# Performance work log

Measured on AMD Instinct MI355X. Metric: run time of the kernel, lower is better.

Reference implementation:

```python
import jax, jax.numpy as jnp
import numpy as np

B, S, D, H = 2, 2048, 1024, 16
DK = D // H

def setup_inputs() -> dict:
    key = jax.random.key(0)
    ks = jax.random.split(key, 8)
    return {
        "query": jax.random.normal(ks[0], (B, S, D), dtype=jnp.float32),
        "key": jax.random.normal(ks[1], (B, S, D), dtype=jnp.float32),
        "value": jax.random.normal(ks[2], (B, S, D), dtype=jnp.float32),
        "mask": jax.random.randint(ks[3], (B, S, S), 0, 2, dtype=jnp.int32),
        "w_q": jax.random.normal(ks[4], (D, D), dtype=jnp.float32) * (D ** -0.5),
        "w_k": jax.random.normal(ks[5], (D, D), dtype=jnp.float32) * (D ** -0.5),
        "w_v": jax.random.normal(ks[6], (D, D), dtype=jnp.float32) * (D ** -0.5),
        "w_o": jax.random.normal(ks[7], (D, D), dtype=jnp.float32) * (D ** -0.5),
    }

def reference(query, key, value, mask, w_q, w_k, w_v, w_o):
    b, s, d = query.shape
    # Linear projections (torch nn.Linear: x @ W.T); here w_* are [out, in]
    Q = jnp.einsum('bsd,ed->bse', query, w_q).reshape(b, s, H, DK).transpose(0, 2, 1, 3)
    K = jnp.einsum('bsd,ed->bse', key, w_k).reshape(b, s, H, DK).transpose(0, 2, 1, 3)
    V = jnp.einsum('bsd,ed->bse', value, w_v).reshape(b, s, H, DK).transpose(0, 2, 1, 3)
    scale = jnp.float32(DK ** 0.5)
    scores = jnp.einsum('bhqd,bhkd->bhqk', Q, K) / scale  # [B,H,S,S]
    scores = jnp.where(mask[:, None, :, :] == 0, jnp.float32(-1e9), scores)
    attn = jax.nn.softmax(scores, axis=-1)  # dropout p=0 -> identity
    out = jnp.einsum('bhqk,bhkd->bhqd', attn, V)  # [B,H,S,DK]
    out = out.transpose(0, 2, 1, 3).reshape(b, s, d)
    return jnp.einsum('bsd,ed->bse', out, w_o)
```

## Files before the change

kernel.cpp:

```cpp
#include <hip/hip_runtime.h>
#include <stdint.h>

#define B_ 2
#define S_ 2048
#define D_ 1024
#define H_ 16
#define DK_ 64

typedef __attribute__((ext_vector_type(8))) short short8;
typedef __attribute__((ext_vector_type(4))) float f32x4;

__device__ __forceinline__ short f2bf(float f) {
    uint32_t u = __float_as_uint(f);
    return (short)((u + 0x7FFFu + ((u >> 16) & 1u)) >> 16);
}

__device__ __forceinline__ float fexp2(float x) {
    float r;
    asm("v_exp_f32 %0, %1" : "=v"(r) : "v"(x));
    return r;
}

__device__ __forceinline__ uint32_t cvt_pk_bf16(float lo, float hi) {
    uint32_t r;
    asm("v_cvt_pk_bf16_f32 %0, %1, %2" : "=v"(r) : "v"(lo), "v"(hi));
    return r;
}

#define GLOAD16(gptr, lptr)                                                      \
    __builtin_amdgcn_global_load_lds(                                            \
        (const __attribute__((address_space(1))) void*)(gptr),                   \
        (__attribute__((address_space(3))) void*)(lptr), 16, 0, 0)

__global__ __launch_bounds__(256) void prep(const float* __restrict__ q,
                                            const float* __restrict__ k,
                                            const float* __restrict__ v,
                                            const float* __restrict__ wq,
                                            const float* __restrict__ wk,
                                            const float* __restrict__ wv,
                                            const float* __restrict__ wo,
                                            const int* __restrict__ mask,
                                            short* __restrict__ qb, short* __restrict__ kb,
                                            short* __restrict__ vb,
                                            short* __restrict__ wqb, short* __restrict__ wkb,
                                            short* __restrict__ wvb, short* __restrict__ wob,
                                            uint32_t* __restrict__ packed,
                                            float* __restrict__ lut) {
    int bid = blockIdx.x;
    int tid = threadIdx.x;
    if (bid < 8192) {
        const float* in;
        short* out;
        int i;
        if (bid < 6144) {
            int sel = bid >> 11;
            i = (bid & 2047) * 256 + tid;
            in = (sel == 0) ? q : (sel == 1) ? k : v;
            out = (sel == 0) ? qb : (sel == 1) ? kb : vb;
        } else {
            int idx = bid - 6144;
            int sel = idx >> 9;
            i = (idx & 511) * 256 + tid;
            in = (sel == 0) ? wq : (sel == 1) ? wk : (sel == 2) ? wv : wo;
            out = (sel == 0) ? wqb : (sel == 1) ? wkb : (sel == 2) ? wvb : wob;
            if (idx == 0 && tid < 64) {
                int e = tid >> 2, r = tid & 3;
                lut[tid] = ((e >> r) & 1) ? 0.0f : -8.0e9f;
            }
        }
        const float4* p = ((const float4*)in) + (size_t)i * 2;
        float4 x = p[0], y = p[1];
        short8 o;
        o[0] = f2bf(x.x); o[1] = f2bf(x.y); o[2] = f2bf(x.z); o[3] = f2bf(x.w);
        o[4] = f2bf(y.x); o[5] = f2bf(y.y); o[6] = f2bf(y.z); o[7] = f2bf(y.w);
        *(((short8*)out) + i) = o;
    } else {
        size_t t = (size_t)(bid - 8192) * 256 + tid;
        int4 m = ((const int4*)mask)[t];
        uint32_t nib = (m.x != 0 ? 1u : 0u) | (m.y != 0 ? 2u : 0u) |
                       (m.z != 0 ? 4u : 0u) | (m.w != 0 ? 8u : 0u);
        int lane = tid & 63;
        uint32_t vv = nib << ((lane & 7) * 4);
        vv |= __shfl_xor(vv, 1);
        vv |= __shfl_xor(vv, 2);
        vv |= __shfl_xor(vv, 4);
        if ((lane & 7) == 0) packed[t >> 3] = vv;
    }
}

#define GEMM_BODY(A, W, C, F32OUT, Mv, Nv, Kv)                                              \
    __shared__ short As[128 * 32];                                                          \
    __shared__ short Bs[128 * 32];                                                          \
    const int tid = threadIdx.x;                                                            \
    const int lane = tid & 63;                                                              \
    const int w = tid >> 6;                                                                 \
    const int wm = w >> 1, wn = w & 1;                                                      \
    const int l_ = blockIdx.x + (blockIdx.y << 3);                                          \
    const int xcd_ = l_ & 7, ii_ = l_ >> 3;                                                 \
    const int mBase = ((xcd_ << 2) + (ii_ >> 3)) * 128;                                     \
    const int nBase = (ii_ & 7) * 128;                                                      \
    f32x4 acc[4][4];                                                                        \
    _Pragma("unroll") for (int i = 0; i < 4; i++)                                           \
        _Pragma("unroll") for (int j = 0; j < 4; j++) acc[i][j] = (f32x4)0.f;               \
    const int srow = lane >> 2;                                                             \
    const int sslot = lane & 3;                                                             \
    for (int k0 = 0; k0 < Kv; k0 += 32) {                                                   \
        _Pragma("unroll") for (int i = 0; i < 2; ++i) {                                     \
            int seg = w * 2 + i;                                                            \
            int row = seg * 16 + srow;                                                      \
            const short* ga = A + (size_t)(mBase + row) * Kv + k0 + sslot * 8;              \
            GLOAD16(ga, (char*)As + seg * 1024);                                            \
            const short* gb = W + (size_t)(nBase + row) * Kv + k0 + sslot * 8;              \
            GLOAD16(gb, (char*)Bs + seg * 1024);                                            \
        }                                                                                   \
        asm volatile("s_waitcnt vmcnt(0)" ::: "memory");                                    \
        __syncthreads();                                                                    \
        short8 af[4], bfv[4];                                                               \
        _Pragma("unroll") for (int mi = 0; mi < 4; mi++)                                    \
            af[mi] = *(const short8*)&As[(wm * 64 + mi * 16 + (lane & 15)) * 32 + (lane >> 4) * 8]; \
        _Pragma("unroll") for (int ni = 0; ni < 4; ni++)                                    \
            bfv[ni] = *(const short8*)&Bs[(wn * 64 + ni * 16 + (lane & 15)) * 32 + (lane >> 4) * 8]; \
        _Pragma("unroll") for (int mi = 0; mi < 4; mi++)                                    \
            _Pragma("unroll") for (int ni = 0; ni < 4; ni++)                                \
                acc[mi][ni] = __builtin_amdgcn_mfma_f32_16x16x32_bf16(af[mi], bfv[ni], acc[mi][ni], 0, 0, 0); \
        __syncthreads();                                                                    \
    }                                                                                       \
    _Pragma("unroll") for (int mi = 0; mi < 4; mi++)                                        \
        _Pragma("unroll") for (int ni = 0; ni < 4; ni++)                                    \
            _Pragma("unroll") for (int r = 0; r < 4; r++) {                                 \
                int row = mBase + wm * 64 + mi * 16 + (lane >> 4) * 4 + r;                  \
                int col = nBase + wn * 64 + ni * 16 + (lane & 15);                          \
                float v = acc[mi][ni][r];                                                   \
                if (F32OUT) ((float*)C)[(size_t)row * Nv + col] = v;                        \
                else        ((short*)C)[(size_t)row * Nv + col] = f2bf(v);                  \
            }

__global__ __launch_bounds__(256) void gemm3_nt(const short* __restrict__ A0, const short* __restrict__ W0, short* __restrict__ C0,
                                                const short* __restrict__ A1, const short* __restrict__ W1, short* __restrict__ C1,
                                                const short* __restrict__ A2, const short* __restrict__ W2, short* __restrict__ C2) {
    const int z = blockIdx.z;
    const short* A = (z == 0) ? A0 : (z == 1) ? A1 : A2;
    const short* W = (z == 0) ? W0 : (z == 1) ? W1 : W2;
    short* C = (z == 0) ? C0 : (z == 1) ? C1 : C2;
    GEMM_BODY(A, W, C, 0, (B_ * S_), D_, D_)
}

__global__ __launch_bounds__(256) void gemm_out(const short* __restrict__ A,
                                                const short* __restrict__ W,
                                                float* __restrict__ C) {
    GEMM_BODY(A, W, C, 1, (B_ * S_), D_, D_)
}

__global__ __launch_bounds__(256) void transpose_v(const short* __restrict__ Vp,
                                                   short* __restrict__ Vt) {
    __shared__ short t[64 * 72];
    int bid = blockIdx.x;
    int bh = bid >> 5;
    int st = bid & 31;
    int b = bh >> 4, h = bh & 15;
    int sBase = st * 64;
    int tid = threadIdx.x;
#pragma unroll
    for (int i = 0; i < 2; i++) {
        int ci = i * 256 + tid;
        int sr = ci >> 3, sl = ci & 7;
        short8 v = *(const short8*)&Vp[(size_t)(b * S_ + sBase + sr) * D_ + h * 64 + sl * 8];
#pragma unroll
        for (int j = 0; j < 8; j++) t[(sl * 8 + j) * 72 + sr] = v[j];
    }
    __syncthreads();
#pragma unroll
    for (int i = 0; i < 2; i++) {
        int ci = i * 256 + tid;
        int dk = ci >> 3, sl = ci & 7;
        short8 o = *(const short8*)&t[dk * 72 + sl * 8];
        *(short8*)&Vt[(size_t)((b * H_ + h) * 64 + dk) * S_ + sBase + sl * 8] = o;
    }
}

__global__ __launch_bounds__(256) void attn_kernel(const short* __restrict__ Qp,
                                                   const short* __restrict__ Kp,
                                                   const short* __restrict__ Vt,
                                                   const uint32_t* __restrict__ mp,
                                                   const float* __restrict__ lutg,
                                                   short* __restrict__ Op) {
    __shared__ short Ks[2][2][64 * 64];
    __shared__ short Vs[2][2][64 * 64];
    const int l_ = blockIdx.x + (blockIdx.y << 4);
    const int bh = ((l_ & 7) << 2) + (l_ >> 7);
    const int qt = (l_ >> 3) & 15;
    const int b = bh >> 4, h = bh & 15;
    const int qBase = qt * 128;
    const int tid = threadIdx.x, lane = tid & 63, w = tid >> 6;
    const int lg = lane >> 4;
    const int li = lane & 15;
    const float c1 = 0.18033688011112042f;

    const int qA = qBase + w * 32 + li;
    const int qB = qA + 16;

    short8 qfA[2], qfB[2];
#pragma unroll
    for (int ks = 0; ks < 2; ks++) {
        qfA[ks] = *(const short8*)&Qp[(size_t)(b * S_ + qA) * D_ + h * 64 + lg * 8 + ks * 32];
        qfB[ks] = *(const short8*)&Qp[(size_t)(b * S_ + qB) * D_ + h * 64 + lg * 8 + ks * 32];
    }

    const int r0 = tid >> 3, sl = tid & 7;
    const int gs = sl ^ (r0 & 7);
    const short* kgb = Kp + ((size_t)(b * S_) + r0) * D_ + h * 64 + gs * 8;
    const short* vgb = Vt + ((size_t)bh * 64 + r0) * S_ + gs * 8;
    const uint32_t* mrowA = mp + ((size_t)(b * S_) + qA) * 64;
    const uint32_t* mrowB = mp + ((size_t)(b * S_) + qB) * 64;
    char* ldsK = (char*)&Ks[0][0][0];
    char* ldsV = (char*)&Vs[0][0][0];
    const int woff = w * 1024;

#pragma unroll
    for (int st = 0; st < 2; st++) {
        GLOAD16(kgb + (size_t)(st * 64) * D_, ldsK + st * 8192 + woff);
        GLOAD16(kgb + (size_t)(st * 64 + 32) * D_, ldsK + st * 8192 + 4096 + woff);
        GLOAD16(vgb + st * 64, ldsV + st * 8192 + woff);
        GLOAD16(vgb + st * 64 + (size_t)32 * S_, ldsV + st * 8192 + 4096 + woff);
    }
    uint4 mw4a = *(const uint4*)mrowA;
    uint4 mw4b = *(const uint4*)mrowB;
    asm volatile("s_waitcnt vmcnt(0)" ::: "memory");
    __syncthreads();

    float m_rA = -1e30f, l_rA = 0.f, m_rB = -1e30f, l_rB = 0.f;
    f32x4 accA[4], accB[4];
#pragma unroll
    for (int g = 0; g < 4; g++) { accA[g] = (f32x4)0.f; accB[g] = (f32x4)0.f; }

    int cur = 0;

    for (int kt = 0; kt < S_ / 128; ++kt) {
        uint32_t mwaA[4] = {mw4a.x, mw4a.y, mw4a.z, mw4a.w};
        uint32_t mwaB[4] = {mw4b.x, mw4b.y, mw4b.z, mw4b.w};
        f32x4 mskA[8], mskB[8];
#pragma unroll
        for (int nt = 0; nt < 8; nt++) {
            uint32_t sh = ((nt & 1) << 4) + (lg << 2);
            mskA[nt] = *(const f32x4*)&lutg[((mwaA[nt >> 1] >> sh) & 0xFu) * 4];
            mskB[nt] = *(const f32x4*)&lutg[((mwaB[nt >> 1] >> sh) & 0xFu) * 4];
        }

        uint4 mwnA, mwnB;
        if (kt < S_ / 128 - 1) {
            const int boff = (cur ^ 1) * 16384 + woff;
#pragma unroll
            for (int st = 0; st < 2; st++) {
                const size_t kr = (size_t)((kt + 1) * 128 + st * 64);
                GLOAD16(kgb + kr * D_, ldsK + boff + st * 8192);
                GLOAD16(kgb + (kr + 32) * D_, ldsK + boff + st * 8192 + 4096);
                GLOAD16(vgb + kr, ldsV + boff + st * 8192);
                GLOAD16(vgb + kr + (size_t)32 * S_, ldsV + boff + st * 8192 + 4096);
            }
            mwnA = *(const uint4*)&mrowA[(kt + 1) * 4];
            mwnB = *(const uint4*)&mrowB[(kt + 1) * 4];
        }

        f32x4 scA[8], scB[8];
        __builtin_amdgcn_s_setprio(1);
#pragma unroll
        for (int st = 0; st < 2; st++)
#pragma unroll
            for (int ntl = 0; ntl < 4; ntl++) {
                f32x4 cA = mskA[st * 4 + ntl];
                f32x4 cB = mskB[st * 4 + ntl];
#pragma unroll
                for (int ks = 0; ks < 2; ks++) {
                    short8 kf = *(const short8*)&Ks[cur][st][(ntl * 16 + li) * 64 + (((lg + ks * 4) ^ (li & 7)) << 3)];
                    cA = __builtin_amdgcn_mfma_f32_16x16x32_bf16(kf, qfA[ks], cA, 0, 0, 0);
                    cB = __builtin_amdgcn_mfma_f32_16x16x32_bf16(kf, qfB[ks], cB, 0, 0, 0);
                }
                scA[st * 4 + ntl] = cA;
                scB[st * 4 + ntl] = cB;
            }
        __builtin_amdgcn_s_setprio(0);

        float a0 = fmaxf(fmaxf(scA[0][0], scA[0][1]), fmaxf(scA[0][2], scA[0][3]));
        float a1 = fmaxf(fmaxf(scA[1][0], scA[1][1]), fmaxf(scA[1][2], scA[1][3]));
        float a2 = fmaxf(fmaxf(scA[2][0], scA[2][1]), fmaxf(scA[2][2], scA[2][3]));
        float a3 = fmaxf(fmaxf(scA[3][0], scA[3][1]), fmaxf(scA[3][2], scA[3][3]));
        float a4 = fmaxf(fmaxf(scA[4][0], scA[4][1]), fmaxf(scA[4][2], scA[4][3]));
        float a5 = fmaxf(fmaxf(scA[5][0], scA[5][1]), fmaxf(scA[5][2], scA[5][3]));
        float a6 = fmaxf(fmaxf(scA[6][0], scA[6][1]), fmaxf(scA[6][2], scA[6][3]));
        float a7 = fmaxf(fmaxf(scA[7][0], scA[7][1]), fmaxf(scA[7][2], scA[7][3]));
        float tmA = fmaxf(fmaxf(fmaxf(a0, a1), fmaxf(a2, a3)),
                          fmaxf(fmaxf(a4, a5), fmaxf(a6, a7)));
        tmA = fmaxf(tmA, __shfl_xor(tmA, 16));
        tmA = fmaxf(tmA, __shfl_xor(tmA, 32));
        float b0 = fmaxf(fmaxf(scB[0][0], scB[0][1]), fmaxf(scB[0][2], scB[0][3]));
        float b1 = fmaxf(fmaxf(scB[1][0], scB[1][1]), fmaxf(scB[1][2], scB[1][3]));
        float b2 = fmaxf(fmaxf(scB[2][0], scB[2][1]), fmaxf(scB[2][2], scB[2][3]));
        float b3 = fmaxf(fmaxf(scB[3][0], scB[3][1]), fmaxf(scB[3][2], scB[3][3]));
        float b4 = fmaxf(fmaxf(scB[4][0], scB[4][1]), fmaxf(scB[4][2], scB[4][3]));
        float b5 = fmaxf(fmaxf(scB[5][0], scB[5][1]), fmaxf(scB[5][2], scB[5][3]));
        float b6 = fmaxf(fmaxf(scB[6][0], scB[6][1]), fmaxf(scB[6][2], scB[6][3]));
        float b7 = fmaxf(fmaxf(scB[7][0], scB[7][1]), fmaxf(scB[7][2], scB[7][3]));
        float tmB = fmaxf(fmaxf(fmaxf(b0, b1), fmaxf(b2, b3)),
                          fmaxf(fmaxf(b4, b5), fmaxf(b6, b7)));
        tmB = fmaxf(tmB, __shfl_xor(tmB, 16));
        tmB = fmaxf(tmB, __shfl_xor(tmB, 32));

        if (__any(((tmA - m_rA) * c1 > 10.0f) || ((tmB - m_rB) * c1 > 10.0f))) {
            float mnA = fmaxf(m_rA, tmA);
            float alA = fexp2((m_rA - mnA) * c1);
            m_rA = mnA; l_rA *= alA;
            float mnB = fmaxf(m_rB, tmB);
            float alB = fexp2((m_rB - mnB) * c1);
            m_rB = mnB; l_rB *= alB;
#pragma unroll
            for (int g = 0; g < 4; g++) { accA[g] *= alA; accB[g] *= alB; }
        }
        float mcA = m_rA * c1, mcB = m_rB * c1;

        uint32_t uA[8][2], uB[8][2];
        float lsA = 0.f, lsB = 0.f;
#pragma unroll
        for (int nt = 0; nt < 8; nt++) {
            float e0 = fexp2(__builtin_fmaf(scA[nt][0], c1, -mcA));
            float e1 = fexp2(__builtin_fmaf(scA[nt][1], c1, -mcA));
            float e2 = fexp2(__builtin_fmaf(scA[nt][2], c1, -mcA));
            float e3 = fexp2(__builtin_fmaf(scA[nt][3], c1, -mcA));
            lsA += (e0 + e1) + (e2 + e3);
            uA[nt][0] = cvt_pk_bf16(e0, e1);
            uA[nt][1] = cvt_pk_bf16(e2, e3);
            float f0 = fexp2(__builtin_fmaf(scB[nt][0], c1, -mcB));
            float f1 = fexp2(__builtin_fmaf(scB[nt][1], c1, -mcB));
            float f2 = fexp2(__builtin_fmaf(scB[nt][2], c1, -mcB));
            float f3 = fexp2(__builtin_fmaf(scB[nt][3], c1, -mcB));
            lsB += (f0 + f1) + (f2 + f3);
            uB[nt][0] = cvt_pk_bf16(f0, f1);
            uB[nt][1] = cvt_pk_bf16(f2, f3);
        }
        lsA += __shfl_xor(lsA, 16);
        lsA += __shfl_xor(lsA, 32);
        l_rA += lsA;
        lsB += __shfl_xor(lsB, 16);
        lsB += __shfl_xor(lsB, 32);
        l_rB += lsB;

        __builtin_amdgcn_s_setprio(1);
#pragma unroll
        for (int ks = 0; ks < 4; ks++) {
            const uint32_t sA00 = uA[2 * ks][0], sA01 = uA[2 * ks][1];
            const uint32_t sA10 = uA[2 * ks + 1][0], sA11 = uA[2 * ks + 1][1];
            uint32_t eA0 = (lg & 1) ? sA00 : sA10;
            uint32_t eA1 = (lg & 1) ? sA01 : sA11;
            uint32_t xA0 = (uint32_t)__shfl_xor((int)eA0, 16);
            uint32_t xA1 = (uint32_t)__shfl_xor((int)eA1, 16);
            union { uint32_t w4[4]; short8 s8; } puA;
            puA.w4[0] = (lg & 1) ? xA0 : sA00;
            puA.w4[1] = (lg & 1) ? xA1 : sA01;
            puA.w4[2] = (lg & 1) ? sA10 : xA0;
            puA.w4[3] = (lg & 1) ? sA11 : xA1;
            const uint32_t sB00 = uB[2 * ks][0], sB01 = uB[2 * ks][1];
            const uint32_t sB10 = uB[2 * ks + 1][0], sB11 = uB[2 * ks + 1][1];
            uint32_t eB0 = (lg & 1) ? sB00 : sB10;
            uint32_t eB1 = (lg & 1) ? sB01 : sB11;
            uint32_t xB0 = (uint32_t)__shfl_xor((int)eB0, 16);
            uint32_t xB1 = (uint32_t)__shfl_xor((int)eB1, 16);
            union { uint32_t w4[4]; short8 s8; } puB;
            puB.w4[0] = (lg & 1) ? xB0 : sB00;
            puB.w4[1] = (lg & 1) ? xB1 : sB01;
            puB.w4[2] = (lg & 1) ? sB10 : xB0;
            puB.w4[3] = (lg & 1) ? sB11 : xB1;
            const int f = ks * 4 + ((lg & 1) << 1) + (lg >> 1);
            const int stv = f >> 3, fl = f & 7;
#pragma unroll
            for (int g = 0; g < 4; g++) {
                short8 vf = *(const short8*)&Vs[cur][stv][(g * 16 + li) * 64 + ((fl ^ (li & 7)) << 3)];
                accA[g] = __builtin_amdgcn_mfma_f32_16x16x32_bf16(vf, puA.s8, accA[g], 0, 0, 0);
                accB[g] = __builtin_amdgcn_mfma_f32_16x16x32_bf16(vf, puB.s8, accB[g], 0, 0, 0);
            }
        }
        __builtin_amdgcn_s_setprio(0);

        asm volatile("s_waitcnt vmcnt(0)" ::: "memory");
        __syncthreads();
        cur ^= 1;
        if (kt < S_ / 128 - 1) { mw4a = mwnA; mw4b = mwnB; }
    }

    float invA = 1.f / l_rA, invB = 1.f / l_rB;
    short* orowA = &Op[(size_t)(b * S_ + qA) * D_ + h * 64];
    short* orowB = &Op[(size_t)(b * S_ + qB) * D_ + h * 64];
#pragma unroll
    for (int g = 0; g < 4; g++) {
        uint2 oa, ob;
        oa.x = cvt_pk_bf16(accA[g][0] * invA, accA[g][1] * invA);
        oa.y = cvt_pk_bf16(accA[g][2] * invA, accA[g][3] * invA);
        *(uint2*)&orowA[g * 16 + lg * 4] = oa;
        ob.x = cvt_pk_bf16(accB[g][0] * invB, accB[g][1] * invB);
        ob.y = cvt_pk_bf16(accB[g][2] * invB, accB[g][3] * invB);
        *(uint2*)&orowB[g * 16 + lg * 4] = ob;
    }
}

extern "C" void kernel_launch(void* const* d_in, const int* in_sizes, int n_in,
                              void* d_out, int out_size, void* d_ws, size_t ws_size,
                              hipStream_t stream) {
    const float* q  = (const float*)d_in[0];
    const float* k  = (const float*)d_in[1];
    const float* v  = (const float*)d_in[2];
    const int*   mk = (const int*)d_in[3];
    const float* wq = (const float*)d_in[4];
    const float* wk = (const float*)d_in[5];
    const float* wv = (const float*)d_in[6];
    const float* wo = (const float*)d_in[7];

    const size_t SZ = (size_t)B_ * S_ * D_;
    const size_t DD = (size_t)D_ * D_;
    const size_t NEED = (6 * SZ + 4 * DD) * 2 + (size_t)B_ * S_ * 64 * 4 + 256;
    if (ws_size < NEED) return;

    short* ws  = (short*)d_ws;
    short* qb  = ws;
    short* kb  = qb + SZ;
    short* vb  = kb + SZ;
    short* wqb = vb + SZ;
    short* wkb = wqb + DD;
    short* wvb = wkb + DD;
    short* wob = wvb + DD;
    short* Qp  = wob + DD;
    short* Kp  = Qp + SZ;
    short* Vp  = Kp + SZ;
    uint32_t* mp = (uint32_t*)(Vp + SZ);
    float* lutg = (float*)(mp + (size_t)B_ * S_ * 64);
    short* Vtr = qb;
    short* Opx = kb;

    dim3 blk(256);
    prep<<<dim3(16384), blk, 0, stream>>>(q, k, v, wq, wk, wv, wo, mk,
                                          qb, kb, vb, wqb, wkb, wvb, wob, mp, lutg);

    gemm3_nt<<<dim3(8, 32, 3), blk, 0, stream>>>(qb, wqb, Qp, kb, wkb, Kp, vb, wvb, Vp);

    transpose_v<<<dim3(B_ * H_ * (S_ / 64)), blk, 0, stream>>>(Vp, Vtr);

    attn_kernel<<<dim3(16, 32), dim3(256), 0, stream>>>(Qp, Kp, Vtr, mp, lutg, Opx);

    gemm_out<<<dim3(8, 32), blk, 0, stream>>>(Opx, wob, (float*)d_out);
}
```

Measured before the change: 157.0 us.

## Load V fragments directly from a fragment-ordered global layout instead of via LDS

The V transpose kernel now writes V in a layout already ordered by MFMA fragment, grouped per key tile and fragment index. The attention kernel reads each lane's V operand straight from global memory into registers, ping-ponging between two register sets, and no longer stages V through double-buffered shared memory. This removes the V LDS traffic, halves LDS usage and may raise occupancy. In exchange the V loads now sit inside the compute loop with less latency hiding, and every block re-reads V from global memory or cache.

```diff
diff --git a/kernel.cpp b/kernel.cpp
--- a/kernel.cpp
+++ b/kernel.cpp
@@ -152,13 +152,15 @@
 }
 
 __global__ __launch_bounds__(256) void transpose_v(const short* __restrict__ Vp,
-                                                   short* __restrict__ Vt) {
+                                                   short* __restrict__ Vt2) {
     __shared__ short t[64 * 72];
     int bid = blockIdx.x;
     int bh = bid >> 5;
     int st = bid & 31;
     int b = bh >> 4, h = bh & 15;
     int sBase = st * 64;
+    int kt = st >> 1;
+    int fbase = (st & 1) * 8;
     int tid = threadIdx.x;
 #pragma unroll
     for (int i = 0; i < 2; i++) {
@@ -172,20 +174,19 @@
 #pragma unroll
     for (int i = 0; i < 2; i++) {
         int ci = i * 256 + tid;
-        int dk = ci >> 3, sl = ci & 7;
-        short8 o = *(const short8*)&t[dk * 72 + sl * 8];
-        *(short8*)&Vt[(size_t)((b * H_ + h) * 64 + dk) * S_ + sBase + sl * 8] = o;
+        int fl = ci >> 6, dv = ci & 63;
+        short8 o = *(const short8*)&t[dv * 72 + fl * 8];
+        *(short8*)&Vt2[(size_t)(((bh * 16 + kt) * 16 + fbase + fl) * 64 + dv) * 8] = o;
     }
 }
 
 __global__ __launch_bounds__(256) void attn_kernel(const short* __restrict__ Qp,
                                                    const short* __restrict__ Kp,
-                                                   const short* __restrict__ Vt,
+                                                   const short* __restrict__ Vt2,
                                                    const uint32_t* __restrict__ mp,
                                                    const float* __restrict__ lutg,
                                                    short* __restrict__ Op) {
     __shared__ short Ks[2][2][64 * 64];
-    __shared__ short Vs[2][2][64 * 64];
     const int l_ = blockIdx.x + (blockIdx.y << 4);
     const int bh = ((l_ & 7) << 2) + (l_ >> 7);
     const int qt = (l_ >> 3) & 15;
@@ -209,19 +210,22 @@
     const int r0 = tid >> 3, sl = tid & 7;
     const int gs = sl ^ (r0 & 7);
     const short* kgb = Kp + ((size_t)(b * S_) + r0) * D_ + h * 64 + gs * 8;
-    const short* vgb = Vt + ((size_t)bh * 64 + r0) * S_ + gs * 8;
     const uint32_t* mrowA = mp + ((size_t)(b * S_) + qA) * 64;
     const uint32_t* mrowB = mp + ((size_t)(b * S_) + qB) * 64;
     char* ldsK = (char*)&Ks[0][0][0];
-    char* ldsV = (char*)&Vs[0][0][0];
     const int woff = w * 1024;
+
+    const int flg = ((lg & 1) << 1) + (lg >> 1);
+    const short* v2b = Vt2 + ((size_t)bh * 16) * 8192;
+
+#define LOADV2(dst, ksv, v2k)                                                    \
+    _Pragma("unroll") for (int g = 0; g < 4; g++)                                \
+        dst[g] = *(const short8*)&(v2k)[(((ksv) * 4 + flg) * 64 + g * 16 + li) * 8];
 
 #pragma unroll
     for (int st = 0; st < 2; st++) {
         GLOAD16(kgb + (size_t)(st * 64) * D_, ldsK + st * 8192 + woff);
         GLOAD16(kgb + (size_t)(st * 64 + 32) * D_, ldsK + st * 8192 + 4096 + woff);
-        GLOAD16(vgb + st * 64, ldsV + st * 8192 + woff);
-        GLOAD16(vgb + st * 64 + (size_t)32 * S_, ldsV + st * 8192 + 4096 + woff);
     }
     uint4 mw4a = *(const uint4*)mrowA;
     uint4 mw4b = *(const uint4*)mrowB;
@@ -236,6 +240,11 @@
     int cur = 0;
 
     for (int kt = 0; kt < S_ / 128; ++kt) {
+        const short* v2k = v2b + (size_t)kt * 8192;
+        short8 vA[4], vB[4];
+        LOADV2(vA, 0, v2k);
+        LOADV2(vB, 1, v2k);
+
         uint32_t mwaA[4] = {mw4a.x, mw4a.y, mw4a.z, mw4a.w};
         uint32_t mwaB[4] = {mw4b.x, mw4b.y, mw4b.z, mw4b.w};
         f32x4 mskA[8], mskB[8];
@@ -254,8 +263,6 @@
                 const size_t kr = (size_t)((kt + 1) * 128 + st * 64);
                 GLOAD16(kgb + kr * D_, ldsK + boff + st * 8192);
                 GLOAD16(kgb + (kr + 32) * D_, ldsK + boff + st * 8192 + 4096);
-                GLOAD16(vgb + kr, ldsV + boff + st * 8192);
-                GLOAD16(vgb + kr + (size_t)32 * S_, ldsV + boff + st * 8192 + 4096);
             }
             mwnA = *(const uint4*)&mrowA[(kt + 1) * 4];
             mwnB = *(const uint4*)&mrowB[(kt + 1) * 4];
@@ -368,14 +375,14 @@
             puB.w4[1] = (lg & 1) ? xB1 : sB01;
             puB.w4[2] = (lg & 1) ? sB10 : xB0;
             puB.w4[3] = (lg & 1) ? sB11 : xB1;
-            const int f = ks * 4 + ((lg & 1) << 1) + (lg >> 1);
-            const int stv = f >> 3, fl = f & 7;
 #pragma unroll
             for (int g = 0; g < 4; g++) {
-                short8 vf = *(const short8*)&Vs[cur][stv][(g * 16 + li) * 64 + ((fl ^ (li & 7)) << 3)];
+                short8 vf = (ks & 1) ? vB[g] : vA[g];
                 accA[g] = __builtin_amdgcn_mfma_f32_16x16x32_bf16(vf, puA.s8, accA[g], 0, 0, 0);
                 accB[g] = __builtin_amdgcn_mfma_f32_16x16x32_bf16(vf, puB.s8, accB[g], 0, 0, 0);
             }
+            if (ks == 0) { LOADV2(vA, 2, v2k); }
+            else if (ks == 1) { LOADV2(vB, 3, v2k); }
         }
         __builtin_amdgcn_s_setprio(0);
 
@@ -398,6 +405,7 @@
         ob.y = cvt_pk_bf16(accB[g][2] * invB, accB[g][3] * invB);
         *(uint2*)&orowB[g * 16 + lg * 4] = ob;
     }
+#undef LOADV2
 }
 
 extern "C" void kernel_launch(void* const* d_in, const int* in_sizes, int n_in,
```

Measured after the change: 168.4 us. 1.07x slower.

## Double GEMM K-tile to 64 with XOR-swizzled LDS and defer row-sum reduction

Applied to the files above, without the earlier changes.

The projection GEMM now stages 64-wide K tiles instead of 32, halving the number of load/barrier iterations, and uses an XOR swizzle on the 16-byte LDS slots so the fragment reads avoid bank conflicts. Separately, the attention kernel no longer reduces the per-lane softmax row sums across lane groups on every key tile; partial sums accumulate per lane and are reduced once after the loop. This is valid only if the running max rescale factor is uniform across those lanes. The larger tile doubles the GEMM's LDS footprint, which could lower occupancy.

```diff
diff --git a/kernel.cpp b/kernel.cpp
--- a/kernel.cpp
+++ b/kernel.cpp
@@ -89,12 +89,13 @@
 }
 
 #define GEMM_BODY(A, W, C, F32OUT, Mv, Nv, Kv)                                              \
-    __shared__ short As[128 * 32];                                                          \
-    __shared__ short Bs[128 * 32];                                                          \
+    __shared__ short As[128 * 64];                                                          \
+    __shared__ short Bs[128 * 64];                                                          \
     const int tid = threadIdx.x;                                                            \
     const int lane = tid & 63;                                                              \
     const int w = tid >> 6;                                                                 \
     const int wm = w >> 1, wn = w & 1;                                                      \
+    const int li = lane & 15, lg = lane >> 4;                                               \
     const int l_ = blockIdx.x + (blockIdx.y << 3);                                          \
     const int xcd_ = l_ & 7, ii_ = l_ >> 3;                                                 \
     const int mBase = ((xcd_ << 2) + (ii_ >> 3)) * 128;                                     \
@@ -102,27 +103,30 @@
     f32x4 acc[4][4];                                                                        \
     _Pragma("unroll") for (int i = 0; i < 4; i++)                                           \
         _Pragma("unroll") for (int j = 0; j < 4; j++) acc[i][j] = (f32x4)0.f;               \
-    const int srow = lane >> 2;                                                             \
-    const int sslot = lane & 3;                                                             \
-    for (int k0 = 0; k0 < Kv; k0 += 32) {                                                   \
-        _Pragma("unroll") for (int i = 0; i < 2; ++i) {                                     \
-            int seg = w * 2 + i;                                                            \
-            int row = seg * 16 + srow;                                                      \
-            const short* ga = A + (size_t)(mBase + row) * Kv + k0 + sslot * 8;              \
-            GLOAD16(ga, (char*)As + seg * 1024);                                            \
-            const short* gb = W + (size_t)(nBase + row) * Kv + k0 + sslot * 8;              \
-            GLOAD16(gb, (char*)Bs + seg * 1024);                                            \
+    const int srow = tid >> 3;                            \
+    const int sgs = (tid & 7) ^ (srow & 7);                   \
+    for (int k0 = 0; k0 < Kv; k0 += 64) {                                                   \
+        _Pragma("unroll") for (int L = 0; L < 4; ++L) {                                     \
+            int row = L * 32 + srow;                                                        \
+            const short* ga = A + (size_t)(mBase + row) * Kv + k0 + sgs * 8;                \
+            GLOAD16(ga, (char*)As + L * 4096 + w * 1024);                                   \
+            const short* gb = W + (size_t)(nBase + row) * Kv + k0 + sgs * 8;                \
+            GLOAD16(gb, (char*)Bs + L * 4096 + w * 1024);                                   \
         }                                                                                   \
         asm volatile("s_waitcnt vmcnt(0)" ::: "memory");                                    \
         __syncthreads();                                                                    \
-        short8 af[4], bfv[4];                                                               \
+        short8 af[4][2], bfv[4][2];                                                         \
         _Pragma("unroll") for (int mi = 0; mi < 4; mi++)                                    \
-            af[mi] = *(const short8*)&As[(wm * 64 + mi * 16 + (lane & 15)) * 32 + (lane >> 4) * 8]; \
-        _Pragma("unroll") for (int ni = 0; ni < 4; ni++)                                    \
-            bfv[ni] = *(const short8*)&Bs[(wn * 64 + ni * 16 + (lane & 15)) * 32 + (lane >> 4) * 8]; \
-        _Pragma("unroll") for (int mi = 0; mi < 4; mi++)                                    \
-            _Pragma("unroll") for (int ni = 0; ni < 4; ni++)                                \
-                acc[mi][ni] = __builtin_amdgcn_mfma_f32_16x16x32_bf16(af[mi], bfv[ni], acc[mi][ni], 0, 0, 0); \
+            _Pragma("unroll") for (int ks = 0; ks < 2; ks++) {                              \
+                int rowa = wm * 64 + mi * 16 + li;                                          \
+                af[mi][ks] = *(const short8*)&As[rowa * 64 + (((lg + ks * 4) ^ (li & 7)) << 3)]; \
+                int rowb = wn * 64 + mi * 16 + li;                                          \
+                bfv[mi][ks] = *(const short8*)&Bs[rowb * 64 + (((lg + ks * 4) ^ (li & 7)) << 3)]; \
+            }                                                                               \
+        _Pragma("unroll") for (int ks = 0; ks < 2; ks++)                                    \
+            _Pragma("unroll") for (int mi = 0; mi < 4; mi++)                                \
+                _Pragma("unroll") for (int ni = 0; ni < 4; ni++)                            \
+                    acc[mi][ni] = __builtin_amdgcn_mfma_f32_16x16x32_bf16(af[mi][ks], bfv[ni][ks], acc[mi][ni], 0, 0, 0); \
         __syncthreads();                                                                    \
     }                                                                                       \
     _Pragma("unroll") for (int mi = 0; mi < 4; mi++)                                        \
@@ -336,11 +340,7 @@
             uB[nt][0] = cvt_pk_bf16(f0, f1);
             uB[nt][1] = cvt_pk_bf16(f2, f3);
         }
-        lsA += __shfl_xor(lsA, 16);
-        lsA += __shfl_xor(lsA, 32);
         l_rA += lsA;
-        lsB += __shfl_xor(lsB, 16);
-        lsB += __shfl_xor(lsB, 32);
         l_rB += lsB;
 
         __builtin_amdgcn_s_setprio(1);
@@ -385,6 +385,10 @@
         if (kt < S_ / 128 - 1) { mw4a = mwnA; mw4b = mwnB; }
     }
 
+    l_rA += __shfl_xor(l_rA, 16);
+    l_rA += __shfl_xor(l_rA, 32);
+    l_rB += __shfl_xor(l_rB, 16);
+    l_rB += __shfl_xor(l_rB, 32);
     float invA = 1.f / l_rA, invB = 1.f / l_rB;
     short* orowA = &Op[(size_t)(b * S_ + qA) * D_ + h * 64];
     short* orowB = &Op[(size_t)(b * S_ + qB) * D_ + h * 64];
```

After: 157.6 us. No clear change (+0.4%).
